# Kernel optimization log

Hardware: AMD Instinct MI355X
Metric: run time of the kernel (lower is better)

## Reference

```python
import jax, jax.numpy as jnp
import numpy as np

N, E, F_IN, HID, HEADS, NCLS = 50000, 800000, 512, 64, 4, 40
NEG_SLOPE = 0.2


def setup_inputs() -> dict:
    key = jax.random.key(0)
    ks = jax.random.split(key, 12)
    x = jax.random.normal(ks[0], (N, F_IN), jnp.float32)
    edge_index = jax.random.randint(ks[1], (2, E), 0, N, jnp.int32)
    edge_weight = jnp.ones((E,), jnp.float32)
    s1 = 1.0 / np.sqrt(F_IN)
    s2 = 1.0 / np.sqrt(HID * HEADS)
    return {
        "x": x,
        "edge_index": edge_index,
        "edge_weight": edge_weight,
        "W1": jax.random.normal(ks[2], (F_IN, HEADS * HID), jnp.float32) * s1,
        "a_src1": jax.random.normal(ks[3], (HEADS, HID), jnp.float32) * s1,
        "a_dst1": jax.random.normal(ks[4], (HEADS, HID), jnp.float32) * s1,
        "b1": jnp.zeros((HEADS * HID,), jnp.float32),
        "W2": jax.random.normal(ks[5], (HEADS * HID, NCLS), jnp.float32) * s2,
        "a_src2": jax.random.normal(ks[6], (1, NCLS), jnp.float32) * s2,
        "a_dst2": jax.random.normal(ks[7], (1, NCLS), jnp.float32) * s2,
        "b2": jnp.zeros((NCLS,), jnp.float32),
    }


def _gat_layer(x, src, dst, ew, W, a_s, a_d, b, heads, n):
    c = W.shape[1] // heads
    h = (x @ W).reshape(n, heads, c)                      # [N,H,C]
    alpha_s = jnp.einsum('nhc,hc->nh', h, a_s)            # [N,H]
    alpha_d = jnp.einsum('nhc,hc->nh', h, a_d)
    e = jax.nn.leaky_relu(alpha_s[src] + alpha_d[dst], NEG_SLOPE)  # [Et,H]
    # segment softmax over destination nodes (self-loops guarantee nonempty segs)
    m = jax.ops.segment_max(e, dst, num_segments=n)
    ex = jnp.exp(e - m[dst])
    denom = jax.ops.segment_sum(ex, dst, num_segments=n)
    alpha = ex / (denom[dst] + 1e-16)                     # [Et,H]
    alpha = alpha * ew[:, None]
    msg = h[src] * alpha[:, :, None]                      # [Et,H,C]
    out = jax.ops.segment_sum(msg, dst, num_segments=n)   # [N,H,C]
    return out.reshape(n, heads * c) + b


def reference(x, edge_index, edge_weight, W1, a_src1, a_dst1, b1, W2, a_src2, a_dst2, b2):
    n = x.shape[0]
    loop = jnp.arange(n, dtype=edge_index.dtype)
    src = jnp.concatenate([edge_index[0], loop])
    dst = jnp.concatenate([edge_index[1], loop])
    ew = jnp.concatenate([edge_weight, jnp.ones((n,), edge_weight.dtype)])
    h = _gat_layer(x, src, dst, ew, W1, a_src1, a_dst1, b1, HEADS, n)
    h = jax.nn.relu(h)  # dropout p=0.0, eval mode: no-op
    out = _gat_layer(h, src, dst, ew, W2, a_src2, a_dst2, b2, 1, n)
    return out  # Identity (log_softmax_return=False)
```

## Files before the change

### kernel.cpp

```cpp
#include <hip/hip_runtime.h>
#include <math.h>

#define N_NODES 50000
#define N_EDGES 800000
#define ET (N_EDGES + N_NODES)
#define F_IN 512
#define HID 64
#define HEADS 4
#define C1 (HEADS * HID)
#define NCLS 40
#define NEG_SLOPE 0.2f

#define BUK_SHIFT 7
#define BUK_NODES (1 << BUK_SHIFT)
#define NBUK ((N_NODES + BUK_NODES - 1) / BUK_NODES)
#define CAP 4096
#define NREP 4
#define SUBCAP (CAP / NREP)
#define BF_STRIDE 8
#define EPB_A 2048
#define NBLK_A ((ET + EPB_A - 1) / EPB_A)
#define RCAP 2560

typedef __attribute__((ext_vector_type(8))) short short8;
typedef __attribute__((ext_vector_type(4))) float floatx4;

__device__ __forceinline__ float leaky(float x) { return fmaxf(x, NEG_SLOPE * x); }

__device__ __forceinline__ unsigned short f2bf(float f) {
    unsigned u = __float_as_uint(f);
    u += 0x7fffu + ((u >> 16) & 1u);
    return (unsigned short)(u >> 16);
}
__device__ __forceinline__ float bf2f(unsigned short u) {
    return __uint_as_float(((unsigned)u) << 16);
}
__device__ __forceinline__ float bflo(unsigned v) { return __uint_as_float(v << 16); }
__device__ __forceinline__ float bfhi(unsigned v) { return __uint_as_float(v & 0xffff0000u); }

__device__ __forceinline__ void edge_sd(int e, const int* __restrict__ ei,
                                        const float* __restrict__ ew,
                                        int& s, int& d, float& w) {
    if (e < N_EDGES) { s = ei[e]; d = ei[N_EDGES + e]; w = ew[e]; }
    else             { s = d = e - N_EDGES; w = 1.f; }
}

__global__ __launch_bounds__(256) void passA_kernel(const int* __restrict__ ei,
                                                    const float* __restrict__ ew,
                                                    int* __restrict__ bfill,
                                                    int2* __restrict__ SB) {
    __shared__ int lcnt[NBUK];
    __shared__ int lbase[NBUK];
    const int t = threadIdx.x;
    const int rep = blockIdx.x & (NREP - 1);
    const int e0 = blockIdx.x * EPB_A + t;
    for (int i = t; i < NBUK; i += 256) lcnt[i] = 0;
    __syncthreads();
    int rx[8], ry[8];
    #pragma unroll
    for (int i = 0; i < 8; i++) {
        int e = e0 + i * 256;
        rx[i] = -1;
        ry[i] = 0;
        if (e < ET) {
            int s, d; float w;
            edge_sd(e, ei, ew, s, d, w);
            rx[i] = s | (d << 16);
            ry[i] = __float_as_int(w);
            atomicAdd(&lcnt[d >> BUK_SHIFT], 1);
        }
    }
    __syncthreads();
    for (int i = t; i < NBUK; i += 256) {
        int c = lcnt[i];
        lbase[i] = c ? atomicAdd(&bfill[(i * NREP + rep) * BF_STRIDE], c) : 0;
        lcnt[i] = 0;
    }
    __syncthreads();
    #pragma unroll
    for (int i = 0; i < 8; i++) {
        if (rx[i] != -1) {
            int b = ((unsigned)rx[i] >> 16) >> BUK_SHIFT;
            int r = atomicAdd(&lcnt[b], 1);
            int idx = lbase[b] + r;
            if (idx < SUBCAP)
                SB[(size_t)b * CAP + rep * SUBCAP + idx] = make_int2(rx[i], ry[i]);
        }
    }
}

__global__ __launch_bounds__(512) void scan_bbase_kernel(const int* __restrict__ bfill,
                                                         int* __restrict__ bbase) {
    __shared__ int sm[512];
    int t = threadIdx.x;
    int v = 0;
    if (t < NBUK) {
        #pragma unroll
        for (int r = 0; r < NREP; r++) {
            int c = bfill[(t * NREP + r) * BF_STRIDE];
            v += (c > SUBCAP) ? SUBCAP : c;
        }
    }
    sm[t] = v;
    __syncthreads();
    #pragma unroll
    for (int s = 1; s < 512; s <<= 1) {
        int u = (t >= s) ? sm[t - s] : 0;
        __syncthreads();
        sm[t] += u;
        __syncthreads();
    }
    if (t < NBUK) bbase[t] = sm[t] - v;
}

__global__ __launch_bounds__(512) void place_kernel(const int* __restrict__ bfill,
                                                    const int* __restrict__ bbase,
                                                    const int2* __restrict__ SB,
                                                    int* __restrict__ row_ptr,
                                                    int2* __restrict__ E2) {
    __shared__ int2 rec[RCAP];
    __shared__ int lh[BUK_NODES];
// ... 17 lines not shown
    for (int r = 0; r < NREP; r++) {
        const int2* base = SB + (size_t)b * CAP + r * SUBCAP;
        for (int i = t; i < c[r]; i += 512) {
            int idx = off[r] + i;
            if (idx < RCAP) rec[idx] = base[i];
        }
    }
    if (tot > RCAP) tot = RCAP;
    __syncthreads();
    for (int i = t; i < tot; i += 512)
        atomicAdd(&lh[(((unsigned)rec[i].x) >> 16) - n0], 1);
    __syncthreads();
    if (t < BUK_NODES) excl[t] = lh[t];
    __syncthreads();
    #pragma unroll
    for (int s = 1; s < BUK_NODES; s <<= 1) {
        int u = (t < BUK_NODES && t >= s) ? excl[t - s] : 0;
        __syncthreads();
        if (t < BUK_NODES) excl[t] += u;
        __syncthreads();
    }
    const int base_b = bbase[b];
    if (t < BUK_NODES) {
        int e = excl[t] - lh[t];
        int node = n0 + t;
        if (node < N_NODES) row_ptr[node] = base_b + e;
        lh[t] = e;
    }
    __syncthreads();
    for (int i = t; i < tot; i += 512) {
        int2 v = rec[i];
        int d = (((unsigned)v.x) >> 16) - n0;
        int pos = atomicAdd(&lh[d], 1);
        E2[base_b + pos] = make_int2(v.x & 0xffff, v.y);
    }
}

__global__ void wt_prep_kernel(const float* __restrict__ W, unsigned short* __restrict__ WT) {
    __shared__ float tile[32][33];
    int k0 = blockIdx.x * 32;
    int n0 = blockIdx.y * 32;
    int tx = threadIdx.x, ty = threadIdx.y;
    #pragma unroll
    for (int i = 0; i < 32; i += 8)
        tile[ty + i][tx] = W[(size_t)(k0 + ty + i) * C1 + n0 + tx];
    __syncthreads();
    #pragma unroll
    for (int i = 0; i < 32; i += 8)
        WT[(size_t)(n0 + ty + i) * F_IN + k0 + tx] = f2bf(tile[tx][ty + i]);
}

__global__ __launch_bounds__(512) void gemm1_mfma_kernel(const float* __restrict__ X,
                                                         const unsigned short* __restrict__ WT,
                                                         const float* __restrict__ a_s1,
                                                         const float* __restrict__ a_d1,
                                                         unsigned short* __restrict__ H,
                                                         float* __restrict__ AS,
                                                         float* __restrict__ AD) {
    __shared__ short As[128][40];
    __shared__ short Bs[256][40];
    const int t = threadIdx.x;
    const int m0 = blockIdx.x * 128;
    const int lane = t & 63;
    const int wave = t >> 6;
    const int wm = wave >> 2;
    const int wn = wave & 3;
    const int l15 = lane & 15;
    const int quad = lane >> 4;

    const int ar = t >> 2;
    const int ac0 = (t & 3) * 8;
    const int gr = m0 + ar;
    const int bn = t >> 1;
    const int bc0 = (t & 1) * 16;

    floatx4 acc[4][4];
    #pragma unroll
    for (int i = 0; i < 4; i++)
        #pragma unroll
        for (int j = 0; j < 4; j++) acc[i][j] = (floatx4){0.f, 0.f, 0.f, 0.f};

    for (int k0 = 0; k0 < F_IN; k0 += 32) {
        float xv[8];
        if (gr < N_NODES) {
            const float4* p = (const float4*)(X + (size_t)gr * F_IN + k0 + ac0);
            float4 v0 = p[0], v1 = p[1];
            xv[0] = v0.x; xv[1] = v0.y; xv[2] = v0.z; xv[3] = v0.w;
            xv[4] = v1.x; xv[5] = v1.y; xv[6] = v1.z; xv[7] = v1.w;
        } else {
            #pragma unroll
            for (int i = 0; i < 8; i++) xv[i] = 0.f;
        }
        short8 av;
        #pragma unroll
        for (int i = 0; i < 8; i++) av[i] = (short)f2bf(xv[i]);
        *(short8*)&As[ar][ac0] = av;

        const short8* q = (const short8*)(WT + (size_t)bn * F_IN + k0 + bc0);
        *(short8*)&Bs[bn][bc0]     = q[0];
        *(short8*)&Bs[bn][bc0 + 8] = q[1];
        __syncthreads();

        short8 a[4], b[4];
        #pragma unroll
        for (int i = 0; i < 4; i++)
            a[i] = *(const short8*)&As[wm * 64 + i * 16 + l15][quad * 8];
        #pragma unroll
        for (int j = 0; j < 4; j++)
            b[j] = *(const short8*)&Bs[wn * 64 + j * 16 + l15][quad * 8];
        #pragma unroll
        for (int i = 0; i < 4; i++)
            #pragma unroll
            for (int j = 0; j < 4; j++)
                acc[i][j] = __builtin_amdgcn_mfma_f32_16x16x32_bf16(a[i], b[j], acc[i][j], 0, 0, 0);
        __syncthreads();
    }

    float asr[4], adr[4];
    #pragma unroll
    for (int j = 0; j < 4; j++) {
        asr[j] = a_s1[wn * HID + j * 16 + l15];
        adr[j] = a_d1[wn * HID + j * 16 + l15];
    }

    #pragma unroll
    for (int i = 0; i < 4; i++) {
        int rbase = m0 + wm * 64 + i * 16 + quad * 4;
        #pragma unroll
        for (int j = 0; j < 4; j++) {
            int col = wn * 64 + j * 16 + l15;
            #pragma unroll
            for (int r = 0; r < 4; r++) {
                int row = rbase + r;
                if (row < N_NODES) H[(size_t)row * C1 + col] = f2bf(acc[i][j][r]);
            }
        }
        #pragma unroll
        for (int r = 0; r < 4; r++) {
            int row = rbase + r;
            float s_ = acc[i][0][r] * asr[0] + acc[i][1][r] * asr[1]
                     + acc[i][2][r] * asr[2] + acc[i][3][r] * asr[3];
            float d_ = acc[i][0][r] * adr[0] + acc[i][1][r] * adr[1]
                     + acc[i][2][r] * adr[2] + acc[i][3][r] * adr[3];
            #pragma unroll
            for (int m = 8; m; m >>= 1) { s_ += __shfl_xor(s_, m); d_ += __shfl_xor(d_, m); }
            if (l15 == 0 && row < N_NODES) {
                AS[row * 4 + wn] = s_;
                AD[row * 4 + wn] = d_;
            }
        }
    }
}

__global__ __launch_bounds__(256) void agg1_csr_kernel(const int* __restrict__ row_ptr,
                                                       const int2* __restrict__ E2,
                                                       const float* __restrict__ AS,
                                                       const float* __restrict__ AD,
                                                       const unsigned short* __restrict__ H,
                                                       const float* __restrict__ b1,
                                                       unsigned short* __restrict__ OUT) {
    int n = blockIdx.x * 4 + (threadIdx.x >> 6);
    int lane = threadIdx.x & 63;
    if (n >= N_NODES) return;
    int l15 = lane & 15;
    int h = lane >> 4;
    int c0 = lane * 4;
    int beg = row_ptr[n];
    int end = (n + 1 < N_NODES) ? row_ptr[n + 1] : ET;
    float ad = AD[n * 4 + h];
    float den = 0.f;
    float a0 = 0.f, a1 = 0.f, a2 = 0.f, a3 = 0.f;

    for (int base = beg; base < end; base += 16) {
        int m = end - base; if (m > 16) m = 16;
        float pw = 0.f; int s = 0;
        if (l15 < m) {
            int2 e = E2[base + l15];
            s = e.x;
            float pe = __expf(leaky(AS[e.x * 4 + h] + ad));
            den += pe;
            pw = pe * __int_as_float(e.y);
        }
        int p = 0;
        for (; p + 4 <= m; p += 4) {
            int s0 = __shfl(s, p);
            int s1 = __shfl(s, p + 1);
            int s2 = __shfl(s, p + 2);
            int s3 = __shfl(s, p + 3);
            uint2 u0 = *(const uint2*)(H + (size_t)s0 * C1 + c0);
            uint2 u1 = *(const uint2*)(H + (size_t)s1 * C1 + c0);
            uint2 u2 = *(const uint2*)(H + (size_t)s2 * C1 + c0);
            uint2 u3 = *(const uint2*)(H + (size_t)s3 * C1 + c0);
            float w0 = __shfl(pw, h * 16 + p);
            float w1 = __shfl(pw, h * 16 + p + 1);
            float w2 = __shfl(pw, h * 16 + p + 2);
            float w3 = __shfl(pw, h * 16 + p + 3);
            a0 += w0 * bflo(u0.x) + w1 * bflo(u1.x) + w2 * bflo(u2.x) + w3 * bflo(u3.x);
            a1 += w0 * bfhi(u0.x) + w1 * bfhi(u1.x) + w2 * bfhi(u2.x) + w3 * bfhi(u3.x);
            a2 += w0 * bflo(u0.y) + w1 * bflo(u1.y) + w2 * bflo(u2.y) + w3 * bflo(u3.y);
            a3 += w0 * bfhi(u0.y) + w1 * bfhi(u1.y) + w2 * bfhi(u2.y) + w3 * bfhi(u3.y);
        }
        for (; p < m; p++) {
            int s0 = __shfl(s, p);
            uint2 u0 = *(const uint2*)(H + (size_t)s0 * C1 + c0);
            float w0 = __shfl(pw, h * 16 + p);
            a0 += w0 * bflo(u0.x);
            a1 += w0 * bfhi(u0.x);
            a2 += w0 * bflo(u0.y);
            a3 += w0 * bfhi(u0.y);
        }
    }
    den += __shfl_xor(den, 1);
    den += __shfl_xor(den, 2);
    den += __shfl_xor(den, 4);
    den += __shfl_xor(den, 8);

    float r = 1.f / (den + 1e-16f);
    float4 bv = *(const float4*)(b1 + c0);
    float v0 = a0 * r + bv.x, v1 = a1 * r + bv.y, v2 = a2 * r + bv.z, v3 = a3 * r + bv.w;
    v0 = v0 > 0.f ? v0 : 0.f;
    v1 = v1 > 0.f ? v1 : 0.f;
    v2 = v2 > 0.f ? v2 : 0.f;
    v3 = v3 > 0.f ? v3 : 0.f;
    uint2 o;
    o.x = ((unsigned)f2bf(v1) << 16) | (unsigned)f2bf(v0);
    o.y = ((unsigned)f2bf(v3) << 16) | (unsigned)f2bf(v2);
    *(uint2*)(OUT + (size_t)n * C1 + c0) = o;
}

#define BROW 264
__global__ __launch_bounds__(512) void gemm2_mfma_kernel(const unsigned short* __restrict__ A,
                                                         const float* __restrict__ W2,
                                                         const float* __restrict__ a_s2,
                                                         const float* __restrict__ a_d2,
                                                         unsigned short* __restrict__ H2b,
                                                         float* __restrict__ AS2,
                                                         float* __restrict__ AD2) {
    __shared__ short As[256][40];
    __shared__ short Bs[48 * BROW];
    const int t = threadIdx.x;
    const int m0 = blockIdx.x * 256;
    const int lane = t & 63;
    const int wave = t >> 6;
    const int l15 = lane & 15;
    const int quad = lane >> 4;

    for (int i = t; i < 48 * 256; i += 512) {
        int n = i >> 8, k = i & 255;
        float v = (n < NCLS) ? W2[k * NCLS + n] : 0.f;
        Bs[n * BROW + k] = (short)f2bf(v);
    }

    const int ar = t >> 1;
    const int ac0 = (t & 1) * 16;

    floatx4 acc[2][3];
    #pragma unroll
    for (int i = 0; i < 2; i++)
        #pragma unroll
        for (int j = 0; j < 3; j++) acc[i][j] = (floatx4){0.f, 0.f, 0.f, 0.f};

    for (int k0 = 0; k0 < C1; k0 += 32) {
        const short8* q = (const short8*)(A + (size_t)(m0 + ar) * C1 + k0 + ac0);
        short8 v0 = q[0], v1 = q[1];
        __syncthreads();
        *(short8*)&As[ar][ac0]     = v0;
        *(short8*)&As[ar][ac0 + 8] = v1;
        __syncthreads();

        short8 a[2], b[3];
        #pragma unroll
        for (int i = 0; i < 2; i++)
            a[i] = *(const short8*)&As[wave * 32 + i * 16 + l15][quad * 8];
        #pragma unroll
        for (int j = 0; j < 3; j++)
            b[j] = *(const short8*)&Bs[(j * 16 + l15) * BROW + k0 + quad * 8];
        #pragma unroll
        for (int i = 0; i < 2; i++)
            #pragma unroll
            for (int j = 0; j < 3; j++)
                acc[i][j] = __builtin_amdgcn_mfma_f32_16x16x32_bf16(a[i], b[j], acc[i][j], 0, 0, 0);
    }

    float asr[3], adr[3];
    #pragma unroll
    for (int j = 0; j < 3; j++) {
        int col = j * 16 + l15;
        asr[j] = (col < NCLS) ? a_s2[col] : 0.f;
        adr[j] = (col < NCLS) ? a_d2[col] : 0.f;
    }

    #pragma unroll
    for (int i = 0; i < 2; i++) {
        #pragma unroll
        for (int r = 0; r < 4; r++) {
            int row = m0 + wave * 32 + i * 16 + quad * 4 + r;
            float s_ = acc[i][0][r] * asr[0] + acc[i][1][r] * asr[1] + acc[i][2][r] * asr[2];
            float d_ = acc[i][0][r] * adr[0] + acc[i][1][r] * adr[1] + acc[i][2][r] * adr[2];
            #pragma unroll
            for (int m = 8; m; m >>= 1) { s_ += __shfl_xor(s_, m); d_ += __shfl_xor(d_, m); }
            if (l15 == 0 && row < N_NODES) { AS2[row] = s_; AD2[row] = d_; }
            #pragma unroll
            for (int j = 0; j < 3; j++) {
                int col = j * 16 + l15;
                if (col < NCLS && row < N_NODES)
                    H2b[(size_t)row * NCLS + col] = f2bf(acc[i][j][r]);
            }
        }
    }
}

__global__ __launch_bounds__(256) void agg2_csr_kernel(const int* __restrict__ row_ptr,
                                                       const int2* __restrict__ E2,
                                                       const float* __restrict__ AS,
                                                       const float* __restrict__ AD,
                                                       const unsigned short* __restrict__ H2b,
                                                       const float* __restrict__ b2,
                                                       float* __restrict__ OUT) {
    int lane = threadIdx.x & 63;
    int n = blockIdx.x * 4 + (threadIdx.x >> 6);
    if (n >= N_NODES) return;
    int beg = row_ptr[n];
    int end = (n + 1 < N_NODES) ? row_ptr[n + 1] : ET;
    float ad = AD[n];
    bool act = lane < NCLS;
    float den = 0.f, acc = 0.f;

    for (int base = beg; base < end; base += 64) {
        int m = end - base; if (m > 64) m = 64;
        float pw = 0.f; int s = 0;
        if (lane < m) {
            int2 e = E2[base + lane];
            s = e.x;
            float pe = __expf(leaky(AS[e.x] + ad));
            den += pe;
            pw = pe * __int_as_float(e.y);
        }
        int p = 0;
        for (; p + 4 <= m; p += 4) {
            int s0 = __shfl(s, p);
            int s1 = __shfl(s, p + 1);
            int s2 = __shfl(s, p + 2);
            int s3 = __shfl(s, p + 3);
            float w0 = __shfl(pw, p);
            float w1 = __shfl(pw, p + 1);
            float w2 = __shfl(pw, p + 2);
            float w3 = __shfl(pw, p + 3);
            if (act) {
                float h0 = bf2f(H2b[(size_t)s0 * NCLS + lane]);
                float h1 = bf2f(H2b[(size_t)s1 * NCLS + lane]);
                float h2 = bf2f(H2b[(size_t)s2 * NCLS + lane]);
                float h3 = bf2f(H2b[(size_t)s3 * NCLS + lane]);
                acc += w0 * h0 + w1 * h1 + w2 * h2 + w3 * h3;
            }
        }
        for (; p < m; p++) {
            int s0 = __shfl(s, p);
            float w0 = __shfl(pw, p);
            if (act) acc += w0 * bf2f(H2b[(size_t)s0 * NCLS + lane]);
        }
    }
    den += __shfl_xor(den, 1);
    den += __shfl_xor(den, 2);
    den += __shfl_xor(den, 4);
    den += __shfl_xor(den, 8);
    den += __shfl_xor(den, 16);
    den += __shfl_xor(den, 32);
    if (act) {
        float r = 1.f / (den + 1e-16f);
        OUT[(size_t)n * NCLS + lane] = acc * r + b2[lane];
    }
}

extern "C" void kernel_launch(void* const* d_in, const int* in_sizes, int n_in,
                              void* d_out, int out_size, void* d_ws, size_t ws_size,
                              hipStream_t stream) {
    const float* x    = (const float*)d_in[0];
    const int*   ei   = (const int*)d_in[1];
    const float* ew   = (const float*)d_in[2];
    const float* W1   = (const float*)d_in[3];
    const float* a_s1 = (const float*)d_in[4];
    const float* a_d1 = (const float*)d_in[5];
    const float* b1   = (const float*)d_in[6];
    const float* W2   = (const float*)d_in[7];
    const float* a_s2 = (const float*)d_in[8];
    const float* a_d2 = (const float*)d_in[9];
    const float* b2   = (const float*)d_in[10];
    float* out = (float*)d_out;

    unsigned short* H1b  = (unsigned short*)d_ws;
    unsigned short* OUT1b = H1b + (size_t)N_NODES * C1;
    float* AS1  = (float*)(OUT1b + (size_t)N_NODES * C1);
    float* AD1  = AS1 + N_NODES * HEADS;
    int* row_ptr = (int*)(AD1 + N_NODES * HEADS);
    int* bfill = row_ptr + N_NODES;
    int* bbase = bfill + NBUK * NREP * BF_STRIDE;
    int2* E2  = (int2*)(bbase + NBUK + 1);
    unsigned short* WT = (unsigned short*)(E2 + ET);
    unsigned short* H2b = H1b;
    float* AS2  = (float*)(H2b + (size_t)N_NODES * NCLS);
    float* AD2  = AS2 + N_NODES;
    int2* SB = (int2*)H1b;

    hipMemsetAsync(bfill, 0, NBUK * NREP * BF_STRIDE * sizeof(int), stream);
    wt_prep_kernel<<<dim3(F_IN / 32, C1 / 32), dim3(32, 8), 0, stream>>>(W1, WT);
    passA_kernel<<<NBLK_A, 256, 0, stream>>>(ei, ew, bfill, SB);
    scan_bbase_kernel<<<1, 512, 0, stream>>>(bfill, bbase);
    place_kernel<<<NBUK, 512, 0, stream>>>(bfill, bbase, SB, row_ptr, E2);

    gemm1_mfma_kernel<<<(N_NODES + 127) / 128, 512, 0, stream>>>(x, WT, a_s1, a_d1, H1b, AS1, AD1);
    agg1_csr_kernel<<<(N_NODES + 3) / 4, 256, 0, stream>>>(row_ptr, E2, AS1, AD1, H1b, b1, OUT1b);

    gemm2_mfma_kernel<<<(N_NODES + 255) / 256, 512, 0, stream>>>(OUT1b, W2, a_s2, a_d2, H2b, AS2, AD2);
    agg2_csr_kernel<<<(N_NODES + 3) / 4, 256, 0, stream>>>(row_ptr, E2, AS2, AD2, H2b, b2, out);
}
```

Before: 330.1 us.

## Split attention weight computation into per-bucket edge kernels and prefetch GEMM tiles

Adds alpha1/alpha2 kernels that compute each edge's exponentiated attention weight once per bucket, accumulate per-node denominators in shared memory, and write per-edge weights to a workspace array. The aggregation kernels then only stream precomputed weights and gather features, with no shuffles or exp work. The GEMM1 loop now prefetches the next X/W tile into registers and converts to bf16 with packed cvt instructions. Packed src/dst edge keys are kept in E2. The extra kernels add launches and roughly 13.6MB of edge-weight traffic in exchange for simpler aggregation loops.

```diff
diff --git a/kernel.cpp b/kernel.cpp
--- a/kernel.cpp
+++ b/kernel.cpp
@@ -170,7 +170,7 @@
         int2 v = rec[i];
         int d = (((unsigned)v.x) >> 16) - n0;
         int pos = atomicAdd(&lh[d], 1);
-        E2[base_b + pos] = make_int2(v.x & 0xffff, v.y);
+        E2[base_b + pos] = v;
     }
 }
 
@@ -211,6 +211,9 @@
     const int gr = m0 + ar;
     const int bn = t >> 1;
     const int bc0 = (t & 1) * 16;
+    const bool rowok = gr < N_NODES;
+    const float4* xp = (const float4*)(X + (size_t)gr * F_IN + ac0);
+    const short8* qp = (const short8*)(WT + (size_t)bn * F_IN + bc0);
 
     floatx4 acc[4][4];
     #pragma unroll
@@ -218,25 +221,27 @@
         #pragma unroll
         for (int j = 0; j < 4; j++) acc[i][j] = (floatx4){0.f, 0.f, 0.f, 0.f};
 
+    float4 v0, v1;
+    short8 wv0, wv1;
+    if (rowok) { v0 = xp[0]; v1 = xp[1]; }
+    else       { v0 = make_float4(0.f,0.f,0.f,0.f); v1 = v0; }
+    wv0 = qp[0]; wv1 = qp[1];
+
     for (int k0 = 0; k0 < F_IN; k0 += 32) {
-        float xv[8];
-        if (gr < N_NODES) {
-            const float4* p = (const float4*)(X + (size_t)gr * F_IN + k0 + ac0);
-            float4 v0 = p[0], v1 = p[1];
-            xv[0] = v0.x; xv[1] = v0.y; xv[2] = v0.z; xv[3] = v0.w;
-            xv[4] = v1.x; xv[5] = v1.y; xv[6] = v1.z; xv[7] = v1.w;
-        } else {
-            #pragma unroll
-            for (int i = 0; i < 8; i++) xv[i] = 0.f;
-        }
-        short8 av;
-        #pragma unroll
-        for (int i = 0; i < 8; i++) av[i] = (short)f2bf(xv[i]);
-        *(short8*)&As[ar][ac0] = av;
-
-        const short8* q = (const short8*)(WT + (size_t)bn * F_IN + k0 + bc0);
-        *(short8*)&Bs[bn][bc0]     = q[0];
-        *(short8*)&Bs[bn][bc0 + 8] = q[1];
+        unsigned r0, r1, r2, r3;
+        asm("v_cvt_pk_bf16_f32 %0, %1, %2" : "=v"(r0) : "v"(v0.x), "v"(v0.y));
+        asm("v_cvt_pk_bf16_f32 %0, %1, %2" : "=v"(r1) : "v"(v0.z), "v"(v0.w));
+        asm("v_cvt_pk_bf16_f32 %0, %1, %2" : "=v"(r2) : "v"(v1.x), "v"(v1.y));
+        asm("v_cvt_pk_bf16_f32 %0, %1, %2" : "=v"(r3) : "v"(v1.z), "v"(v1.w));
+        *(uint4*)&As[ar][ac0] = make_uint4(r0, r1, r2, r3);
+        *(short8*)&Bs[bn][bc0]     = wv0;
+        *(short8*)&Bs[bn][bc0 + 8] = wv1;
+        if (k0 + 32 < F_IN) {
+            int fx = (k0 + 32) >> 2;
+            int sx = (k0 + 32) >> 3;
+            if (rowok) { v0 = xp[fx]; v1 = xp[fx + 1]; }
+            wv0 = qp[sx]; wv1 = qp[sx + 1];
+        }
         __syncthreads();
 
         short8 a[4], b[4];
@@ -290,68 +295,87 @@
     }
 }
 
+__global__ __launch_bounds__(512) void alpha1_kernel(const int* __restrict__ bbase,
+                                                     const int2* __restrict__ E2,
+                                                     const float* __restrict__ AS,
+                                                     const float* __restrict__ AD,
+                                                     float* __restrict__ EW1,
+                                                     float* __restrict__ DEN1) {
+    __shared__ float denS[BUK_NODES * 4];
+    const int b = blockIdx.x;
+    const int n0 = b << BUK_SHIFT;
+    const int t = threadIdx.x;
+    const int beg = bbase[b];
+    const int end = (b == NBUK - 1) ? ET : bbase[b + 1];
+    denS[t] = 0.f;
+    __syncthreads();
+    for (int i = beg + t; i < end; i += 512) {
+        int2 e = E2[i];
+        int s = e.x & 0xffff;
+        int d = ((unsigned)e.x) >> 16;
+        float w = __int_as_float(e.y);
+        float4 as4 = *(const float4*)(AS + s * 4);
+        float4 ad4 = *(const float4*)(AD + d * 4);
+        float p0 = __expf(leaky(as4.x + ad4.x));
+        float p1 = __expf(leaky(as4.y + ad4.y));
+        float p2 = __expf(leaky(as4.z + ad4.z));
+        float p3 = __expf(leaky(as4.w + ad4.w));
+        int dl = (d - n0) * 4;
+        atomicAdd(&denS[dl + 0], p0);
+        atomicAdd(&denS[dl + 1], p1);
+        atomicAdd(&denS[dl + 2], p2);
+        atomicAdd(&denS[dl + 3], p3);
+        *(float4*)(EW1 + (size_t)i * 4) = make_float4(p0 * w, p1 * w, p2 * w, p3 * w);
+    }
+    __syncthreads();
+    int node = n0 + (t >> 2);
+    if (node < N_NODES) DEN1[node * 4 + (t & 3)] = denS[t];
+}
+
 __global__ __launch_bounds__(256) void agg1_csr_kernel(const int* __restrict__ row_ptr,
                                                        const int2* __restrict__ E2,
-                                                       const float* __restrict__ AS,
-                                                       const float* __restrict__ AD,
+                                                       const float* __restrict__ EW1,
+                                                       const float* __restrict__ DEN1,
                                                        const unsigned short* __restrict__ H,
                                                        const float* __restrict__ b1,
                                                        unsigned short* __restrict__ OUT) {
     int n = blockIdx.x * 4 + (threadIdx.x >> 6);
     int lane = threadIdx.x & 63;
     if (n >= N_NODES) return;
-    int l15 = lane & 15;
     int h = lane >> 4;
     int c0 = lane * 4;
-    int beg = row_ptr[n];
-    int end = (n + 1 < N_NODES) ? row_ptr[n + 1] : ET;
-    float ad = AD[n * 4 + h];
-    float den = 0.f;
+    int beg = __builtin_amdgcn_readfirstlane(row_ptr[n]);
+    int end = __builtin_amdgcn_readfirstlane((n + 1 < N_NODES) ? row_ptr[n + 1] : ET);
+    float den = DEN1[n * 4 + h];
     float a0 = 0.f, a1 = 0.f, a2 = 0.f, a3 = 0.f;
 
-    for (int base = beg; base < end; base += 16) {
-        int m = end - base; if (m > 16) m = 16;
-        float pw = 0.f; int s = 0;
-        if (l15 < m) {
-            int2 e = E2[base + l15];
-            s = e.x;
-            float pe = __expf(leaky(AS[e.x * 4 + h] + ad));
-            den += pe;
-            pw = pe * __int_as_float(e.y);
-        }
-        int p = 0;
-        for (; p + 4 <= m; p += 4) {
-            int s0 = __shfl(s, p);
-            int s1 = __shfl(s, p + 1);
-            int s2 = __shfl(s, p + 2);
-            int s3 = __shfl(s, p + 3);
-            uint2 u0 = *(const uint2*)(H + (size_t)s0 * C1 + c0);
-            uint2 u1 = *(const uint2*)(H + (size_t)s1 * C1 + c0);
-            uint2 u2 = *(const uint2*)(H + (size_t)s2 * C1 + c0);
-            uint2 u3 = *(const uint2*)(H + (size_t)s3 * C1 + c0);
-            float w0 = __shfl(pw, h * 16 + p);
-            float w1 = __shfl(pw, h * 16 + p + 1);
-            float w2 = __shfl(pw, h * 16 + p + 2);
-            float w3 = __shfl(pw, h * 16 + p + 3);
-            a0 += w0 * bflo(u0.x) + w1 * bflo(u1.x) + w2 * bflo(u2.x) + w3 * bflo(u3.x);
-            a1 += w0 * bfhi(u0.x) + w1 * bfhi(u1.x) + w2 * bfhi(u2.x) + w3 * bfhi(u3.x);
-            a2 += w0 * bflo(u0.y) + w1 * bflo(u1.y) + w2 * bflo(u2.y) + w3 * bflo(u3.y);
-            a3 += w0 * bfhi(u0.y) + w1 * bfhi(u1.y) + w2 * bfhi(u2.y) + w3 * bfhi(u3.y);
-        }
-        for (; p < m; p++) {
-            int s0 = __shfl(s, p);
-            uint2 u0 = *(const uint2*)(H + (size_t)s0 * C1 + c0);
-            float w0 = __shfl(pw, h * 16 + p);
-            a0 += w0 * bflo(u0.x);
-            a1 += w0 * bfhi(u0.x);
-            a2 += w0 * bflo(u0.y);
-            a3 += w0 * bfhi(u0.y);
-        }
-    }
-    den += __shfl_xor(den, 1);
-    den += __shfl_xor(den, 2);
-    den += __shfl_xor(den, 4);
-    den += __shfl_xor(den, 8);
+    int p = beg;
+    for (; p + 4 <= end; p += 4) {
+        int2 e0 = E2[p], e1 = E2[p + 1], e2 = E2[p + 2], e3 = E2[p + 3];
+        int s0 = e0.x & 0xffff, s1 = e1.x & 0xffff, s2 = e2.x & 0xffff, s3 = e3.x & 0xffff;
+        float w0 = EW1[(size_t)p * 4 + h];
+        float w1 = EW1[(size_t)(p + 1) * 4 + h];
+        float w2 = EW1[(size_t)(p + 2) * 4 + h];
+        float w3 = EW1[(size_t)(p + 3) * 4 + h];
+        uint2 u0 = *(const uint2*)(H + (size_t)s0 * C1 + c0);
+        uint2 u1 = *(const uint2*)(H + (size_t)s1 * C1 + c0);
+        uint2 u2 = *(const uint2*)(H + (size_t)s2 * C1 + c0);
+        uint2 u3 = *(const uint2*)(H + (size_t)s3 * C1 + c0);
+        a0 += w0 * bflo(u0.x) + w1 * bflo(u1.x) + w2 * bflo(u2.x) + w3 * bflo(u3.x);
+        a1 += w0 * bfhi(u0.x) + w1 * bfhi(u1.x) + w2 * bfhi(u2.x) + w3 * bfhi(u3.x);
+        a2 += w0 * bflo(u0.y) + w1 * bflo(u1.y) + w2 * bflo(u2.y) + w3 * bflo(u3.y);
+        a3 += w0 * bfhi(u0.y) + w1 * bfhi(u1.y) + w2 * bfhi(u2.y) + w3 * bfhi(u3.y);
+    }
+    for (; p < end; p++) {
+        int2 e0 = E2[p];
+        int s0 = e0.x & 0xffff;
+        float w0 = EW1[(size_t)p * 4 + h];
+        uint2 u0 = *(const uint2*)(H + (size_t)s0 * C1 + c0);
+        a0 += w0 * bflo(u0.x);
+        a1 += w0 * bfhi(u0.x);
+        a2 += w0 * bflo(u0.y);
+        a3 += w0 * bfhi(u0.y);
+    }
 
     float r = 1.f / (den + 1e-16f);
     float4 bv = *(const float4*)(b1 + c0);
@@ -448,62 +472,71 @@
     }
 }
 
+__global__ __launch_bounds__(512) void alpha2_kernel(const int* __restrict__ bbase,
+                                                     const int2* __restrict__ E2,
+                                                     const float* __restrict__ AS,
+                                                     const float* __restrict__ AD,
+                                                     float* __restrict__ EW2,
+                                                     float* __restrict__ DEN2) {
+    __shared__ float denS[BUK_NODES];
+    const int b = blockIdx.x;
+    const int n0 = b << BUK_SHIFT;
+    const int t = threadIdx.x;
+    const int beg = bbase[b];
+    const int end = (b == NBUK - 1) ? ET : bbase[b + 1];
+    if (t < BUK_NODES) denS[t] = 0.f;
+    __syncthreads();
+    for (int i = beg + t; i < end; i += 512) {
+        int2 e = E2[i];
+        int s = e.x & 0xffff;
+        int d = ((unsigned)e.x) >> 16;
+        float w = __int_as_float(e.y);
+        float pe = __expf(leaky(AS[s] + AD[d]));
+        atomicAdd(&denS[d - n0], pe);
+        EW2[i] = pe * w;
+    }
+    __syncthreads();
+    if (t < BUK_NODES) {
+        int node = n0 + t;
+        if (node < N_NODES) DEN2[node] = denS[t];
+    }
+}
+
 __global__ __launch_bounds__(256) void agg2_csr_kernel(const int* __restrict__ row_ptr,
                                                        const int2* __restrict__ E2,
-                                                       const float* __restrict__ AS,
-                                                       const float* __restrict__ AD,
+                                                       const float* __restrict__ EW2,
+                                                       const float* __restrict__ DEN2,
                                                        const unsigned short* __restrict__ H2b,
                                                        const float* __restrict__ b2,
                                                        float* __restrict__ OUT) {
     int lane = threadIdx.x & 63;
     int n = blockIdx.x * 4 + (threadIdx.x >> 6);
     if (n >= N_NODES) return;
-    int beg = row_ptr[n];
-    int end = (n + 1 < N_NODES) ? row_ptr[n + 1] : ET;
-    float ad = AD[n];
+    int beg = __builtin_amdgcn_readfirstlane(row_ptr[n]);
+    int end = __builtin_amdgcn_readfirstlane((n + 1 < N_NODES) ? row_ptr[n + 1] : ET);
+    float den = DEN2[n];
     bool act = lane < NCLS;
-    float den = 0.f, acc = 0.f;
-
-    for (int base = beg; base < end; base += 64) {
-        int m = end - base; if (m > 64) m = 64;
-        float pw = 0.f; int s = 0;
-        if (lane < m) {
-            int2 e = E2[base + lane];
-            s = e.x;
-            float pe = __expf(leaky(AS[e.x] + ad));
-            den += pe;
-            pw = pe * __int_as_float(e.y);
-        }
-        int p = 0;
-        for (; p + 4 <= m; p += 4) {
-            int s0 = __shfl(s, p);
-            int s1 = __shfl(s, p + 1);
-            int s2 = __shfl(s, p + 2);
-            int s3 = __shfl(s, p + 3);
-            float w0 = __shfl(pw, p);
-            float w1 = __shfl(pw, p + 1);
-            float w2 = __shfl(pw, p + 2);
-            float w3 = __shfl(pw, p + 3);
-            if (act) {
-                float h0 = bf2f(H2b[(size_t)s0 * NCLS + lane]);
-                float h1 = bf2f(H2b[(size_t)s1 * NCLS + lane]);
-                float h2 = bf2f(H2b[(size_t)s2 * NCLS + lane]);
-                float h3 = bf2f(H2b[(size_t)s3 * NCLS + lane]);
-                acc += w0 * h0 + w1 * h1 + w2 * h2 + w3 * h3;
-            }
-        }
-        for (; p < m; p++) {
-            int s0 = __shfl(s, p);
-            float w0 = __shfl(pw, p);
-            if (act) acc += w0 * bf2f(H2b[(size_t)s0 * NCLS + lane]);
-        }
-    }
-    den += __shfl_xor(den, 1);
-    den += __shfl_xor(den, 2);
-    den += __shfl_xor(den, 4);
-    den += __shfl_xor(den, 8);
-    den += __shfl_xor(den, 16);
-    den += __shfl_xor(den, 32);
+    float acc = 0.f;
+
+    int p = beg;
+    for (; p + 4 <= end; p += 4) {
+        int2 e0 = E2[p], e1 = E2[p + 1], e2 = E2[p + 2], e3 = E2[p + 3];
+        float w0 = EW2[p], w1 = EW2[p + 1], w2 = EW2[p + 2], w3 = EW2[p + 3];
+        int s0 = e0.x & 0xffff, s1 = e1.x & 0xffff, s2 = e2.x & 0xffff, s3 = e3.x & 0xffff;
+        if (act) {
+            float h0 = bf2f(H2b[(size_t)s0 * NCLS + lane]);
+            float h1 = bf2f(H2b[(size_t)s1 * NCLS + lane]);
+            float h2 = bf2f(H2b[(size_t)s2 * NCLS + lane]);
+            float h3 = bf2f(H2b[(size_t)s3 * NCLS + lane]);
+            acc += w0 * h0 + w1 * h1 + w2 * h2 + w3 * h3;
+        }
+    }
+    for (; p < end; p++) {
+        int2 e0 = E2[p];
+        float w0 = EW2[p];
+        int s0 = e0.x & 0xffff;
+        if (act) acc += w0 * bf2f(H2b[(size_t)s0 * NCLS + lane]);
+    }
     if (act) {
         float r = 1.f / (den + 1e-16f);
         OUT[(size_t)n * NCLS + lane] = acc * r + b2[lane];
@@ -530,14 +563,18 @@
     unsigned short* OUT1b = H1b + (size_t)N_NODES * C1;
     float* AS1  = (float*)(OUT1b + (size_t)N_NODES * C1);
     float* AD1  = AS1 + N_NODES * HEADS;
-    int* row_ptr = (int*)(AD1 + N_NODES * HEADS);
+    float* DEN1 = AD1 + N_NODES * HEADS;
+    int* row_ptr = (int*)(DEN1 + N_NODES * HEADS);
     int* bfill = row_ptr + N_NODES;
     int* bbase = bfill + NBUK * NREP * BF_STRIDE;
     int2* E2  = (int2*)(bbase + NBUK + 1);
-    unsigned short* WT = (unsigned short*)(E2 + ET);
+    float* EW1 = (float*)(E2 + ET);
+    unsigned short* WT = (unsigned short*)(EW1 + (size_t)ET * 4);
     unsigned short* H2b = H1b;
     float* AS2  = (float*)(H2b + (size_t)N_NODES * NCLS);
     float* AD2  = AS2 + N_NODES;
+    float* DEN2 = AD2 + N_NODES;
+    float* EW2  = EW1;
     int2* SB = (int2*)H1b;
 
     hipMemsetAsync(bfill, 0, NBUK * NREP * BF_STRIDE * sizeof(int), stream);
@@ -547,8 +584,10 @@
     place_kernel<<<NBUK, 512, 0, stream>>>(bfill, bbase, SB, row_ptr, E2);
 
     gemm1_mfma_kernel<<<(N_NODES + 127) / 128, 512, 0, stream>>>(x, WT, a_s1, a_d1, H1b, AS1, AD1);
-    agg1_csr_kernel<<<(N_NODES + 3) / 4, 256, 0, stream>>>(row_ptr, E2, AS1, AD1, H1b, b1, OUT1b);
+    alpha1_kernel<<<NBUK, 512, 0, stream>>>(bbase, E2, AS1, AD1, EW1, DEN1);
+    agg1_csr_kernel<<<(N_NODES + 3) / 4, 256, 0, stream>>>(row_ptr, E2, EW1, DEN1, H1b, b1, OUT1b);
 
     gemm2_mfma_kernel<<<(N_NODES + 255) / 256, 512, 0, stream>>>(OUT1b, W2, a_s2, a_d2, H2b, AS2, AD2);
-    agg2_csr_kernel<<<(N_NODES + 3) / 4, 256, 0, stream>>>(row_ptr, E2, AS2, AD2, H2b, b2, out);
-}
+    alpha2_kernel<<<NBUK, 512, 0, stream>>>(bbase, E2, AS2, AD2, EW2, DEN2);
+    agg2_csr_kernel<<<(N_NODES + 3) / 4, 256, 0, stream>>>(row_ptr, E2, EW2, DEN2, H2b, b2, out);
+}
```

Result: slower. 377.5 us (+14.4%).

## Double-buffer gemm1 LDS tiles and split output columns across a second grid dimension

Applied to the files above, without the earlier changes.

The layer-1 GEMM now uses double-buffered LDS tiles and register prefetch, so global loads of the next K-slice overlap the MFMA work on the current one, with one barrier per iteration instead of two. The block is narrowed to 128 output columns with 256 threads, and a second grid dimension covers the two column halves (heads 0-1 and 2-3). This gives twice as many blocks for occupancy. The cost is that X rows are read and converted twice, once per column half. It also switches the fp32-to-bf16 conversion to packed v_cvt_pk_bf16_f32 inline asm.

```diff
diff --git a/kernel.cpp b/kernel.cpp
--- a/kernel.cpp
+++ b/kernel.cpp
@@ -188,29 +188,33 @@
         WT[(size_t)(n0 + ty + i) * F_IN + k0 + tx] = f2bf(tile[tx][ty + i]);
 }
 
-__global__ __launch_bounds__(512) void gemm1_mfma_kernel(const float* __restrict__ X,
+__global__ __launch_bounds__(256) void gemm1_mfma_kernel(const float* __restrict__ X,
                                                          const unsigned short* __restrict__ WT,
                                                          const float* __restrict__ a_s1,
                                                          const float* __restrict__ a_d1,
                                                          unsigned short* __restrict__ H,
                                                          float* __restrict__ AS,
                                                          float* __restrict__ AD) {
-    __shared__ short As[128][40];
-    __shared__ short Bs[256][40];
+    __shared__ short As[2][128][40];
+    __shared__ short Bs[2][128][40];
     const int t = threadIdx.x;
     const int m0 = blockIdx.x * 128;
+    const int cn = blockIdx.y;
     const int lane = t & 63;
     const int wave = t >> 6;
-    const int wm = wave >> 2;
-    const int wn = wave & 3;
+    const int wm = wave >> 1;
+    const int wn = wave & 1;
     const int l15 = lane & 15;
     const int quad = lane >> 4;
 
-    const int ar = t >> 2;
-    const int ac0 = (t & 3) * 8;
+    const int ar = t >> 1;
+    const int ac0 = (t & 1) * 16;
     const int gr = m0 + ar;
+    const bool rowok = gr < N_NODES;
     const int bn = t >> 1;
     const int bc0 = (t & 1) * 16;
+    const float4* xp = (const float4*)(X + (size_t)gr * F_IN + ac0);
+    const short8* qp = (const short8*)(WT + (size_t)(cn * 128 + bn) * F_IN + bc0);
 
     floatx4 acc[4][4];
     #pragma unroll
@@ -218,47 +222,77 @@
         #pragma unroll
         for (int j = 0; j < 4; j++) acc[i][j] = (floatx4){0.f, 0.f, 0.f, 0.f};
 
-    for (int k0 = 0; k0 < F_IN; k0 += 32) {
-        float xv[8];
-        if (gr < N_NODES) {
-            const float4* p = (const float4*)(X + (size_t)gr * F_IN + k0 + ac0);
-            float4 v0 = p[0], v1 = p[1];
-            xv[0] = v0.x; xv[1] = v0.y; xv[2] = v0.z; xv[3] = v0.w;
-            xv[4] = v1.x; xv[5] = v1.y; xv[6] = v1.z; xv[7] = v1.w;
-        } else {
-            #pragma unroll
-            for (int i = 0; i < 8; i++) xv[i] = 0.f;
-        }
-        short8 av;
-        #pragma unroll
-        for (int i = 0; i < 8; i++) av[i] = (short)f2bf(xv[i]);
-        *(short8*)&As[ar][ac0] = av;
-
-        const short8* q = (const short8*)(WT + (size_t)bn * F_IN + k0 + bc0);
-        *(short8*)&Bs[bn][bc0]     = q[0];
-        *(short8*)&Bs[bn][bc0 + 8] = q[1];
-        __syncthreads();
+    float4 xa[4];
+    short8 wb[2];
+    if (rowok) { xa[0] = xp[0]; xa[1] = xp[1]; xa[2] = xp[2]; xa[3] = xp[3]; }
+    else { xa[0] = make_float4(0.f,0.f,0.f,0.f); xa[1] = xa[0]; xa[2] = xa[0]; xa[3] = xa[0]; }
+    wb[0] = qp[0]; wb[1] = qp[1];
+
+    {
+        unsigned r0,r1,r2,r3,r4,r5,r6,r7;
+        asm("v_cvt_pk_bf16_f32 %0, %1, %2" : "=v"(r0) : "v"(xa[0].x), "v"(xa[0].y));
+        asm("v_cvt_pk_bf16_f32 %0, %1, %2" : "=v"(r1) : "v"(xa[0].z), "v"(xa[0].w));
+        asm("v_cvt_pk_bf16_f32 %0, %1, %2" : "=v"(r2) : "v"(xa[1].x), "v"(xa[1].y));
+        asm("v_cvt_pk_bf16_f32 %0, %1, %2" : "=v"(r3) : "v"(xa[1].z), "v"(xa[1].w));
+        asm("v_cvt_pk_bf16_f32 %0, %1, %2" : "=v"(r4) : "v"(xa[2].x), "v"(xa[2].y));
+        asm("v_cvt_pk_bf16_f32 %0, %1, %2" : "=v"(r5) : "v"(xa[2].z), "v"(xa[2].w));
+        asm("v_cvt_pk_bf16_f32 %0, %1, %2" : "=v"(r6) : "v"(xa[3].x), "v"(xa[3].y));
+        asm("v_cvt_pk_bf16_f32 %0, %1, %2" : "=v"(r7) : "v"(xa[3].z), "v"(xa[3].w));
+        *(uint4*)&As[0][ar][ac0]     = make_uint4(r0, r1, r2, r3);
+        *(uint4*)&As[0][ar][ac0 + 8] = make_uint4(r4, r5, r6, r7);
+        *(short8*)&Bs[0][bn][bc0] = wb[0];
+        *(short8*)&Bs[0][bn][bc0 + 8] = wb[1];
+    }
+    __syncthreads();
+
+    int cur = 0;
+    for (int k0 = 32; k0 <= F_IN; k0 += 32) {
+        const bool more = k0 < F_IN;
+        if (more) {
+            int fx = k0 >> 2, sx = k0 >> 3;
+            if (rowok) { xa[0] = xp[fx]; xa[1] = xp[fx+1]; xa[2] = xp[fx+2]; xa[3] = xp[fx+3]; }
+            wb[0] = qp[sx]; wb[1] = qp[sx + 1];
+        }
 
         short8 a[4], b[4];
         #pragma unroll
         for (int i = 0; i < 4; i++)
-            a[i] = *(const short8*)&As[wm * 64 + i * 16 + l15][quad * 8];
+            a[i] = *(const short8*)&As[cur][wm * 64 + i * 16 + l15][quad * 8];
         #pragma unroll
         for (int j = 0; j < 4; j++)
-            b[j] = *(const short8*)&Bs[wn * 64 + j * 16 + l15][quad * 8];
+            b[j] = *(const short8*)&Bs[cur][wn * 64 + j * 16 + l15][quad * 8];
         #pragma unroll
         for (int i = 0; i < 4; i++)
             #pragma unroll
             for (int j = 0; j < 4; j++)
                 acc[i][j] = __builtin_amdgcn_mfma_f32_16x16x32_bf16(a[i], b[j], acc[i][j], 0, 0, 0);
-        __syncthreads();
-    }
-
+
+        if (more) {
+            int nxt = cur ^ 1;
+            unsigned r0,r1,r2,r3,r4,r5,r6,r7;
+            asm("v_cvt_pk_bf16_f32 %0, %1, %2" : "=v"(r0) : "v"(xa[0].x), "v"(xa[0].y));
+            asm("v_cvt_pk_bf16_f32 %0, %1, %2" : "=v"(r1) : "v"(xa[0].z), "v"(xa[0].w));
+            asm("v_cvt_pk_bf16_f32 %0, %1, %2" : "=v"(r2) : "v"(xa[1].x), "v"(xa[1].y));
+            asm("v_cvt_pk_bf16_f32 %0, %1, %2" : "=v"(r3) : "v"(xa[1].z), "v"(xa[1].w));
+            asm("v_cvt_pk_bf16_f32 %0, %1, %2" : "=v"(r4) : "v"(xa[2].x), "v"(xa[2].y));
+            asm("v_cvt_pk_bf16_f32 %0, %1, %2" : "=v"(r5) : "v"(xa[2].z), "v"(xa[2].w));
+            asm("v_cvt_pk_bf16_f32 %0, %1, %2" : "=v"(r6) : "v"(xa[3].x), "v"(xa[3].y));
+            asm("v_cvt_pk_bf16_f32 %0, %1, %2" : "=v"(r7) : "v"(xa[3].z), "v"(xa[3].w));
+            *(uint4*)&As[nxt][ar][ac0]     = make_uint4(r0, r1, r2, r3);
+            *(uint4*)&As[nxt][ar][ac0 + 8] = make_uint4(r4, r5, r6, r7);
+            *(short8*)&Bs[nxt][bn][bc0] = wb[0];
+            *(short8*)&Bs[nxt][bn][bc0 + 8] = wb[1];
+            __syncthreads();
+            cur = nxt;
+        }
+    }
+
+    const int head = cn * 2 + wn;
     float asr[4], adr[4];
     #pragma unroll
     for (int j = 0; j < 4; j++) {
-        asr[j] = a_s1[wn * HID + j * 16 + l15];
-        adr[j] = a_d1[wn * HID + j * 16 + l15];
+        asr[j] = a_s1[head * HID + j * 16 + l15];
+        adr[j] = a_d1[head * HID + j * 16 + l15];
     }
 
     #pragma unroll
@@ -266,7 +300,7 @@
         int rbase = m0 + wm * 64 + i * 16 + quad * 4;
         #pragma unroll
         for (int j = 0; j < 4; j++) {
-            int col = wn * 64 + j * 16 + l15;
+            int col = cn * 128 + wn * 64 + j * 16 + l15;
             #pragma unroll
             for (int r = 0; r < 4; r++) {
                 int row = rbase + r;
@@ -283,8 +317,8 @@
             #pragma unroll
             for (int m = 8; m; m >>= 1) { s_ += __shfl_xor(s_, m); d_ += __shfl_xor(d_, m); }
             if (l15 == 0 && row < N_NODES) {
-                AS[row * 4 + wn] = s_;
-                AD[row * 4 + wn] = d_;
+                AS[row * 4 + head] = s_;
+                AD[row * 4 + head] = d_;
             }
         }
     }
@@ -546,7 +580,7 @@
     scan_bbase_kernel<<<1, 512, 0, stream>>>(bfill, bbase);
     place_kernel<<<NBUK, 512, 0, stream>>>(bfill, bbase, SB, row_ptr, E2);
 
-    gemm1_mfma_kernel<<<(N_NODES + 127) / 128, 512, 0, stream>>>(x, WT, a_s1, a_d1, H1b, AS1, AD1);
+    gemm1_mfma_kernel<<<dim3((N_NODES + 127) / 128, 2), 256, 0, stream>>>(x, WT, a_s1, a_d1, H1b, AS1, AD1);
     agg1_csr_kernel<<<(N_NODES + 3) / 4, 256, 0, stream>>>(row_ptr, E2, AS1, AD1, H1b, b1, OUT1b);
 
     gemm2_mfma_kernel<<<(N_NODES + 255) / 256, 512, 0, stream>>>(OUT1b, W2, a_s2, a_d2, H2b, AS2, AD2);
```

New measurement: 342.2 us. 1.04x slower.

## Fuse edge bucketing into GEMM1 launch and layer-2 projection into aggregation

Applied to the files above, without the earlier changes.

The edge bucketing pass now runs as extra blocks of the layer-1 GEMM launch, so the two independent stages can overlap and one launch is removed. The layer-2 linear projection and attention logits are computed inside the layer-1 aggregation kernel from a per-node vector in shared memory. This avoids writing and re-reading the bf16 hidden activations and drops the separate MFMA GEMM2 kernel. In exchange every aggregation block converts all of W2 into shared memory (20KB) and does the 256x40 product with scalar FMAs instead of matrix cores. That may cost occupancy and adds per-block redundant work.

```diff
diff --git a/kernel.cpp b/kernel.cpp
--- a/kernel.cpp
+++ b/kernel.cpp
@@ -20,6 +20,7 @@
 #define BF_STRIDE 8
 #define EPB_A 2048
 #define NBLK_A ((ET + EPB_A - 1) / EPB_A)
+#define NG1 ((N_NODES + 127) / 128)
 #define RCAP 2560
 
 typedef __attribute__((ext_vector_type(8))) short short8;
@@ -43,50 +44,6 @@
                                         int& s, int& d, float& w) {
     if (e < N_EDGES) { s = ei[e]; d = ei[N_EDGES + e]; w = ew[e]; }
     else             { s = d = e - N_EDGES; w = 1.f; }
-}
-
-__global__ __launch_bounds__(256) void passA_kernel(const int* __restrict__ ei,
-                                                    const float* __restrict__ ew,
-                                                    int* __restrict__ bfill,
-                                                    int2* __restrict__ SB) {
-    __shared__ int lcnt[NBUK];
-    __shared__ int lbase[NBUK];
-    const int t = threadIdx.x;
-    const int rep = blockIdx.x & (NREP - 1);
-    const int e0 = blockIdx.x * EPB_A + t;
-    for (int i = t; i < NBUK; i += 256) lcnt[i] = 0;
-    __syncthreads();
-    int rx[8], ry[8];
-    #pragma unroll
-    for (int i = 0; i < 8; i++) {
-        int e = e0 + i * 256;
-        rx[i] = -1;
-        ry[i] = 0;
-        if (e < ET) {
-            int s, d; float w;
-            edge_sd(e, ei, ew, s, d, w);
-            rx[i] = s | (d << 16);
-            ry[i] = __float_as_int(w);
-            atomicAdd(&lcnt[d >> BUK_SHIFT], 1);
-        }
-    }
-    __syncthreads();
-    for (int i = t; i < NBUK; i += 256) {
-        int c = lcnt[i];
-        lbase[i] = c ? atomicAdd(&bfill[(i * NREP + rep) * BF_STRIDE], c) : 0;
-        lcnt[i] = 0;
-    }
-    __syncthreads();
-    #pragma unroll
-    for (int i = 0; i < 8; i++) {
-        if (rx[i] != -1) {
-            int b = ((unsigned)rx[i] >> 16) >> BUK_SHIFT;
-            int r = atomicAdd(&lcnt[b], 1);
-            int idx = lbase[b] + r;
-            if (idx < SUBCAP)
-                SB[(size_t)b * CAP + rep * SUBCAP + idx] = make_int2(rx[i], ry[i]);
-        }
-    }
 }
 
 __global__ __launch_bounds__(512) void scan_bbase_kernel(const int* __restrict__ bfill,
@@ -188,16 +145,63 @@
         WT[(size_t)(n0 + ty + i) * F_IN + k0 + tx] = f2bf(tile[tx][ty + i]);
 }
 
-__global__ __launch_bounds__(512) void gemm1_mfma_kernel(const float* __restrict__ X,
-                                                         const unsigned short* __restrict__ WT,
-                                                         const float* __restrict__ a_s1,
-                                                         const float* __restrict__ a_d1,
-                                                         unsigned short* __restrict__ H,
-                                                         float* __restrict__ AS,
-                                                         float* __restrict__ AD) {
+__global__ __launch_bounds__(512) void g1pa_kernel(const float* __restrict__ X,
+                                                   const unsigned short* __restrict__ WT,
+                                                   const float* __restrict__ a_s1,
+                                                   const float* __restrict__ a_d1,
+                                                   unsigned short* __restrict__ H,
+                                                   float* __restrict__ AS,
+                                                   float* __restrict__ AD,
+                                                   const int* __restrict__ ei,
+                                                   const float* __restrict__ ew,
+                                                   int* __restrict__ bfill,
+                                                   int2* __restrict__ SB) {
     __shared__ short As[128][40];
     __shared__ short Bs[256][40];
+    __shared__ int lcnt[NBUK];
+    __shared__ int lbase[NBUK];
     const int t = threadIdx.x;
+
+    if (blockIdx.x >= NG1) {
+        const int pb = blockIdx.x - NG1;
+        const int rep = pb & (NREP - 1);
+        const int e0 = pb * EPB_A + t;
+        for (int i = t; i < NBUK; i += 512) lcnt[i] = 0;
+        __syncthreads();
+        int rx[4], ry[4];
+        #pragma unroll
+        for (int i = 0; i < 4; i++) {
+            int e = e0 + i * 512;
+            rx[i] = -1;
+            ry[i] = 0;
+            if (e < ET) {
+                int s, d; float w;
+                edge_sd(e, ei, ew, s, d, w);
+                rx[i] = s | (d << 16);
+                ry[i] = __float_as_int(w);
+                atomicAdd(&lcnt[d >> BUK_SHIFT], 1);
+            }
+        }
+        __syncthreads();
+        for (int i = t; i < NBUK; i += 512) {
+            int c = lcnt[i];
+            lbase[i] = c ? atomicAdd(&bfill[(i * NREP + rep) * BF_STRIDE], c) : 0;
+            lcnt[i] = 0;
+        }
+        __syncthreads();
+        #pragma unroll
+        for (int i = 0; i < 4; i++) {
+            if (rx[i] != -1) {
+                int b = ((unsigned)rx[i] >> 16) >> BUK_SHIFT;
+                int r = atomicAdd(&lcnt[b], 1);
+                int idx = lbase[b] + r;
+                if (idx < SUBCAP)
+                    SB[(size_t)b * CAP + rep * SUBCAP + idx] = make_int2(rx[i], ry[i]);
+            }
+        }
+        return;
+    }
+
     const int m0 = blockIdx.x * 128;
     const int lane = t & 63;
     const int wave = t >> 6;
@@ -290,19 +294,29 @@
     }
 }
 
-__global__ __launch_bounds__(256) void agg1_csr_kernel(const int* __restrict__ row_ptr,
-                                                       const int2* __restrict__ E2,
-                                                       const float* __restrict__ AS,
-                                                       const float* __restrict__ AD,
-                                                       const unsigned short* __restrict__ H,
-                                                       const float* __restrict__ b1,
-                                                       unsigned short* __restrict__ OUT) {
-    int n = blockIdx.x * 4 + (threadIdx.x >> 6);
-    int lane = threadIdx.x & 63;
-    if (n >= N_NODES) return;
-    int l15 = lane & 15;
-    int h = lane >> 4;
-    int c0 = lane * 4;
+__global__ __launch_bounds__(256) void agg1_fused_kernel(const int* __restrict__ row_ptr,
+                                                         const int2* __restrict__ E2,
+                                                         const float* __restrict__ AS,
+                                                         const float* __restrict__ AD,
+                                                         const unsigned short* __restrict__ H,
+                                                         const float* __restrict__ b1,
+                                                         const float* __restrict__ W2,
+                                                         const float* __restrict__ a_s2,
+                                                         const float* __restrict__ a_d2,
+                                                         unsigned short* __restrict__ H2b,
+                                                         float* __restrict__ AS2,
+                                                         float* __restrict__ AD2) {
+    __shared__ short w2s[C1 * NCLS];
+    __shared__ float vsh[4][C1];
+    const int t = threadIdx.x;
+    for (int i = t; i < C1 * NCLS; i += 256) w2s[i] = (short)f2bf(W2[i]);
+
+    const int wave = t >> 6;
+    const int n = blockIdx.x * 4 + wave;
+    const int lane = t & 63;
+    const int l15 = lane & 15;
+    const int h = lane >> 4;
+    const int c0 = lane * 4;
     int beg = row_ptr[n];
     int end = (n + 1 < N_NODES) ? row_ptr[n + 1] : ET;
     float ad = AD[n * 4 + h];
@@ -360,92 +374,28 @@
     v1 = v1 > 0.f ? v1 : 0.f;
     v2 = v2 > 0.f ? v2 : 0.f;
     v3 = v3 > 0.f ? v3 : 0.f;
-    uint2 o;
-    o.x = ((unsigned)f2bf(v1) << 16) | (unsigned)f2bf(v0);
-    o.y = ((unsigned)f2bf(v3) << 16) | (unsigned)f2bf(v2);
-    *(uint2*)(OUT + (size_t)n * C1 + c0) = o;
-}
-
-#define BROW 264
-__global__ __launch_bounds__(512) void gemm2_mfma_kernel(const unsigned short* __restrict__ A,
-                                                         const float* __restrict__ W2,
-                                                         const float* __restrict__ a_s2,
-                                                         const float* __restrict__ a_d2,
-                                                         unsigned short* __restrict__ H2b,
-                                                         float* __restrict__ AS2,
-                                                         float* __restrict__ AD2) {
-    __shared__ short As[256][40];
-    __shared__ short Bs[48 * BROW];
-    const int t = threadIdx.x;
-    const int m0 = blockIdx.x * 256;
-    const int lane = t & 63;
-    const int wave = t >> 6;
-    const int l15 = lane & 15;
-    const int quad = lane >> 4;
-
-    for (int i = t; i < 48 * 256; i += 512) {
-        int n = i >> 8, k = i & 255;
-        float v = (n < NCLS) ? W2[k * NCLS + n] : 0.f;
-        Bs[n * BROW + k] = (short)f2bf(v);
-    }
-
-    const int ar = t >> 1;
-    const int ac0 = (t & 1) * 16;
-
-    floatx4 acc[2][3];
-    #pragma unroll
-    for (int i = 0; i < 2; i++)
-        #pragma unroll
-        for (int j = 0; j < 3; j++) acc[i][j] = (floatx4){0.f, 0.f, 0.f, 0.f};
-
-    for (int k0 = 0; k0 < C1; k0 += 32) {
-        const short8* q = (const short8*)(A + (size_t)(m0 + ar) * C1 + k0 + ac0);
-        short8 v0 = q[0], v1 = q[1];
-        __syncthreads();
-        *(short8*)&As[ar][ac0]     = v0;
-        *(short8*)&As[ar][ac0 + 8] = v1;
-        __syncthreads();
-
-        short8 a[2], b[3];
-        #pragma unroll
-        for (int i = 0; i < 2; i++)
-            a[i] = *(const short8*)&As[wave * 32 + i * 16 + l15][quad * 8];
-        #pragma unroll
-        for (int j = 0; j < 3; j++)
-            b[j] = *(const short8*)&Bs[(j * 16 + l15) * BROW + k0 + quad * 8];
-        #pragma unroll
-        for (int i = 0; i < 2; i++)
-            #pragma unroll
-            for (int j = 0; j < 3; j++)
-                acc[i][j] = __builtin_amdgcn_mfma_f32_16x16x32_bf16(a[i], b[j], acc[i][j], 0, 0, 0);
-    }
-
-    float asr[3], adr[3];
-    #pragma unroll
-    for (int j = 0; j < 3; j++) {
-        int col = j * 16 + l15;
-        asr[j] = (col < NCLS) ? a_s2[col] : 0.f;
-        adr[j] = (col < NCLS) ? a_d2[col] : 0.f;
-    }
-
-    #pragma unroll
-    for (int i = 0; i < 2; i++) {
-        #pragma unroll
-        for (int r = 0; r < 4; r++) {
-            int row = m0 + wave * 32 + i * 16 + quad * 4 + r;
-            float s_ = acc[i][0][r] * asr[0] + acc[i][1][r] * asr[1] + acc[i][2][r] * asr[2];
-            float d_ = acc[i][0][r] * adr[0] + acc[i][1][r] * adr[1] + acc[i][2][r] * adr[2];
-            #pragma unroll
-            for (int m = 8; m; m >>= 1) { s_ += __shfl_xor(s_, m); d_ += __shfl_xor(d_, m); }
-            if (l15 == 0 && row < N_NODES) { AS2[row] = s_; AD2[row] = d_; }
-            #pragma unroll
-            for (int j = 0; j < 3; j++) {
-                int col = j * 16 + l15;
-                if (col < NCLS && row < N_NODES)
-                    H2b[(size_t)row * NCLS + col] = f2bf(acc[i][j][r]);
-            }
-        }
-    }
+    *(float4*)&vsh[wave][c0] = make_float4(v0, v1, v2, v3);
+    __syncthreads();
+
+    const float* vn = vsh[wave];
+    float o = 0.f;
+    if (lane < NCLS) {
+        float o0 = 0.f, o1 = 0.f, o2 = 0.f, o3 = 0.f;
+        #pragma unroll 4
+        for (int c = 0; c < C1; c += 4) {
+            o0 += vn[c]     * bf2f(w2s[c * NCLS + lane]);
+            o1 += vn[c + 1] * bf2f(w2s[(c + 1) * NCLS + lane]);
+            o2 += vn[c + 2] * bf2f(w2s[(c + 2) * NCLS + lane]);
+            o3 += vn[c + 3] * bf2f(w2s[(c + 3) * NCLS + lane]);
+        }
+        o = (o0 + o1) + (o2 + o3);
+    }
+    float s2_ = 0.f, d2_ = 0.f;
+    if (lane < NCLS) { s2_ = o * a_s2[lane]; d2_ = o * a_d2[lane]; }
+    #pragma unroll
+    for (int m = 32; m; m >>= 1) { s2_ += __shfl_xor(s2_, m); d2_ += __shfl_xor(d2_, m); }
+    if (lane == 0) { AS2[n] = s2_; AD2[n] = d2_; }
+    if (lane < NCLS) H2b[(size_t)n * NCLS + lane] = f2bf(o);
 }
 
 __global__ __launch_bounds__(256) void agg2_csr_kernel(const int* __restrict__ row_ptr,
@@ -526,29 +476,30 @@
     const float* b2   = (const float*)d_in[10];
     float* out = (float*)d_out;
 
-    unsigned short* H1b  = (unsigned short*)d_ws;
-    unsigned short* OUT1b = H1b + (size_t)N_NODES * C1;
-    float* AS1  = (float*)(OUT1b + (size_t)N_NODES * C1);
-    float* AD1  = AS1 + N_NODES * HEADS;
-    int* row_ptr = (int*)(AD1 + N_NODES * HEADS);
+    unsigned short* H1b = (unsigned short*)d_ws;
+    float* AS1 = (float*)(H1b + (size_t)N_NODES * C1);
+    float* AD1 = AS1 + N_NODES * HEADS;
+    float* AS2 = AD1 + N_NODES * HEADS;
+    float* AD2 = AS2 + N_NODES;
+    int* row_ptr = (int*)(AD2 + N_NODES);
     int* bfill = row_ptr + N_NODES;
     int* bbase = bfill + NBUK * NREP * BF_STRIDE;
-    int2* E2  = (int2*)(bbase + NBUK + 1);
+    int2* E2 = (int2*)(bbase + NBUK + 1);
     unsigned short* WT = (unsigned short*)(E2 + ET);
-    unsigned short* H2b = H1b;
-    float* AS2  = (float*)(H2b + (size_t)N_NODES * NCLS);
-    float* AD2  = AS2 + N_NODES;
-    int2* SB = (int2*)H1b;
+    int2* SB = (int2*)(WT + (size_t)F_IN * C1);
+    unsigned short* H2b = (unsigned short*)(SB + (size_t)NBUK * CAP);
 
     hipMemsetAsync(bfill, 0, NBUK * NREP * BF_STRIDE * sizeof(int), stream);
     wt_prep_kernel<<<dim3(F_IN / 32, C1 / 32), dim3(32, 8), 0, stream>>>(W1, WT);
-    passA_kernel<<<NBLK_A, 256, 0, stream>>>(ei, ew, bfill, SB);
+
+    g1pa_kernel<<<NG1 + NBLK_A, 512, 0, stream>>>(x, WT, a_s1, a_d1, H1b, AS1, AD1,
+                                                  ei, ew, bfill, SB);
+
     scan_bbase_kernel<<<1, 512, 0, stream>>>(bfill, bbase);
     place_kernel<<<NBUK, 512, 0, stream>>>(bfill, bbase, SB, row_ptr, E2);
 
-    gemm1_mfma_kernel<<<(N_NODES + 127) / 128, 512, 0, stream>>>(x, WT, a_s1, a_d1, H1b, AS1, AD1);
-    agg1_csr_kernel<<<(N_NODES + 3) / 4, 256, 0, stream>>>(row_ptr, E2, AS1, AD1, H1b, b1, OUT1b);
-
-    gemm2_mfma_kernel<<<(N_NODES + 255) / 256, 512, 0, stream>>>(OUT1b, W2, a_s2, a_d2, H2b, AS2, AD2);
+    agg1_fused_kernel<<<N_NODES / 4, 256, 0, stream>>>(row_ptr, E2, AS1, AD1, H1b, b1,
+                                                       W2, a_s2, a_d2, H2b, AS2, AD2);
+
     agg2_csr_kernel<<<(N_NODES + 3) / 4, 256, 0, stream>>>(row_ptr, E2, AS2, AD2, H2b, b2, out);
 }
```

After: 388.1 us. 1.18x slower.
